# Optimization experiments

Hardware: AMD Instinct MI355X
Metric: run time of the kernel (lower is better)

Reference implementation:

```python
import jax, jax.numpy as jnp
import numpy as np

L, B, N, C, H = 8, 8, 512, 1024, 16
D = C // H
TP = (2.0 * D) ** 0.5  # temperature_coeff * head_dim, sqrt


def _ln(x):
    # LayerNorm(eps=1e-6, no affine)
    m = jnp.mean(x, axis=-1, keepdims=True)
    v = jnp.var(x, axis=-1, keepdims=True)
    return (x - m) * jax.lax.rsqrt(v + 1e-6)


def _modulate(x, shift, scale):
    return x * (1 + scale) + shift


def setup_inputs() -> dict:
    key = jax.random.key(0)
    ks = jax.random.split(key, 18)
    s = 0.02
    return {
        "x": jax.random.normal(ks[0], (B, N, C), dtype=jnp.float32),
        "time": jax.random.uniform(ks[1], (B, 1), dtype=jnp.float32) * 100.0,
        "label": jax.random.normal(ks[2], (B, 2), dtype=jnp.float32),
        "x_mask": jax.random.randint(ks[3], (B, N, 1), 0, 2).astype(jnp.float32),
        # ValueLabelEmbed: Linear(2 -> C)
        "Wl": jax.random.normal(ks[4], (C, 2), dtype=jnp.float32) * s,
        "bl": jnp.zeros((C,), dtype=jnp.float32),
        # per-layer stacked weights (leading dim L)
        "Wq": jax.random.normal(ks[5], (L, C, C), dtype=jnp.float32) * s,
        "Wk": jax.random.normal(ks[6], (L, C, C), dtype=jnp.float32) * s,
        "Wv": jax.random.normal(ks[7], (L, C, C), dtype=jnp.float32) * s,
        "W1": jax.random.normal(ks[8], (L, 4 * C, C), dtype=jnp.float32) * s,
        "b1": jnp.zeros((L, 4 * C), dtype=jnp.float32),
        "W2": jax.random.normal(ks[9], (L, C, 4 * C), dtype=jnp.float32) * s,
        "b2": jnp.zeros((L, C), dtype=jnp.float32),
        "Wm": jax.random.normal(ks[10], (L, 6 * C, C), dtype=jnp.float32) * s,
        "bm": jnp.zeros((L, 6 * C), dtype=jnp.float32),
        # FinalLayer
        "Wf": jax.random.normal(ks[11], (C, C), dtype=jnp.float32) * s,
        "bf": jnp.zeros((C,), dtype=jnp.float32),
        "Wmf": jax.random.normal(ks[12], (2 * C, C), dtype=jnp.float32) * s,
        "bmf": jnp.zeros((2 * C,), dtype=jnp.float32),
    }


def reference(x, time, label, x_mask, Wl, bl, Wq, Wk, Wv, W1, b1, W2, b2, Wm, bm, Wf, bf, Wmf, bmf):
    # ValueLabelEmbed: (B,2) -> (B,1,C)
    lemb = (label @ Wl.T + bl)[:, None, :]
    # TimeEmbedding: interleaved sin/cos of time / 10000^(2i/d)
    base = jnp.power(10000.0, 2.0 * jnp.arange(C, dtype=jnp.float32) / C)
    te = time / base  # (B, C)
    even = (jnp.arange(C) % 2) == 0
    te = jnp.where(even, jnp.sin(te), jnp.cos(te))
    c = lemb + te[:, None, :]  # (B,1,C)

    # self-attention mask: True where exactly one of the pair is valid
    xm = x_mask[:, :, 0]  # (B,N)
    mask = ((xm[:, :, None] + xm[:, None, :]) == 1.0)[:, None, :, :]  # (B,1,N,N)

    def block(xc, p):
        wq, wk, wv, w1, bb1, w2, bb2, wm, bbm = p
        m6 = jax.nn.selu(c) @ wm.T + bbm  # (B,1,6C)
        sm, sc, gm, sf, cf, gf = jnp.split(m6, 6, axis=-1)
        h = _modulate(_ln(xc), sm, sc) * x_mask
        q = (h @ wq.T).reshape(B, N, H, D)
        k = (h @ wk.T).reshape(B, N, H, D)
        v = (h @ wv.T).reshape(B, N, H, D)
        scores = jnp.einsum('bqhd,bkhd->bhqk', q, k) / TP
        scores = jnp.where(mask, -jnp.inf, scores)
        alpha = jax.nn.softmax(scores, axis=-1)
        att = jnp.einsum('bhqk,bkhd->bqhd', alpha, v).reshape(B, N, C)
        xc = xc + gm * att
        h2 = _modulate(_ln(xc), sf, cf)
        ffn = jax.nn.selu(h2 @ w1.T + bb1) @ w2.T + bb2
        xc = (xc + gf * ffn) * x_mask
        return xc, None

    x, _ = jax.lax.scan(block, x, (Wq, Wk, Wv, W1, b1, W2, b2, Wm, bm))

    # FinalLayer
    m2 = jax.nn.selu(c) @ Wmf.T + bmf
    shift, scale = jnp.split(m2, 2, axis=-1)
    out = (_modulate(_ln(x), shift, scale) @ Wf.T + bf) * x_mask
    return out
```

## Files before the change

kernel.cpp:

```cpp
#include <hip/hip_runtime.h>
#include <hip/hip_bf16.h>
#include <cstddef>

#define DEVI __device__ __forceinline__

typedef __attribute__((ext_vector_type(4))) float f4v;
typedef __attribute__((ext_vector_type(8))) short s8v;
typedef __attribute__((ext_vector_type(4))) short s4v;

using bf16 = __hip_bfloat16;

constexpr float SELU_A = 1.6732632423543772f;
constexpr float SELU_S = 1.0507009873554805f;
constexpr float TPINV  = 0.08838834764831845f;

DEVI float bfbits(short s) { return __uint_as_float(((unsigned)(unsigned short)s) << 16); }
DEVI unsigned short f2bu(float f) {
  bf16 h = __float2bfloat16(f);
  return __builtin_bit_cast(unsigned short, h);
}
DEVI float seluf(float x) { return x > 0.f ? SELU_S * x : SELU_S * SELU_A * (__expf(x) - 1.f); }

DEVI void gl16(const void* g, void* l) {
  __builtin_amdgcn_global_load_lds((__attribute__((address_space(1))) void*)g,
                                   (__attribute__((address_space(3))) void*)l, 16, 0, 0);
}

__global__ void k_compact(const float* __restrict__ xm, int* __restrict__ idx,
                          int* __restrict__ pos, int* __restrict__ cnt,
                          int* __restrict__ start, int* __restrict__ t2b)
{
  int t = threadIdx.x;
  int b = t >> 6, lane = t & 63;
  __shared__ int scnt[8];
  int base = b * 512 + lane * 8;
  int mb[8]; int lc = 0;
  #pragma unroll
  for (int i = 0; i < 8; i++) { mb[i] = (xm[base + i] != 0.f) ? 1 : 0; lc += mb[i]; }
  int s = lc;
  #pragma unroll
  for (int o = 1; o < 64; o <<= 1) { int tt = __shfl_up(s, o); if (lane >= o) s += tt; }
  int run = s - lc;
  #pragma unroll
  for (int i = 0; i < 8; i++) {
    int n = lane * 8 + i;
    if (mb[i]) { idx[b * 512 + run] = n; pos[b * 512 + n] = run; run++; }
    else pos[b * 512 + n] = -1;
  }
  if (lane == 63) scnt[b] = s;
  __syncthreads();
  if (t == 0) {
    int st = 0, tile = 0;
    for (int bb = 0; bb < 8; bb++) {
      cnt[bb] = scnt[bb];
      start[bb] = st;
      int nt = (scnt[bb] + 127) >> 7;
      for (int k = 0; k < nt; k++) t2b[tile++] = bb;
      st += nt * 128;
    }
    start[8] = st;
    for (; tile < 32; tile++) t2b[tile] = 0;
  }
}

__global__ __launch_bounds__(256) void k_gather(const float* __restrict__ xin,
    const int* __restrict__ idx, const int* __restrict__ cnt,
    const int* __restrict__ start, const int* __restrict__ t2b,
    float* __restrict__ xc)
{
  int row = blockIdx.x, t = threadIdx.x;
  if (row >= start[8]) return;
  int tb = t2b[row >> 7], slot = row - start[tb];
  f4v v = {0.f, 0.f, 0.f, 0.f};
  if (slot < cnt[tb])
    v = *(const f4v*)&xin[((size_t)tb * 512 + idx[tb * 512 + slot]) * 1024 + t * 4];
  *(f4v*)&xc[(size_t)row * 1024 + t * 4] = v;
}

__global__ __launch_bounds__(256) void k_scatter(const float* __restrict__ ffin,
    const int* __restrict__ pos, const int* __restrict__ start, float* __restrict__ out)
{
  int row = blockIdx.x, t = threadIdx.x, b = row >> 9;
  int p = pos[row];
  f4v v = {0.f, 0.f, 0.f, 0.f};
  if (p >= 0) v = *(const f4v*)&ffin[(size_t)(start[b] + p) * 1024 + t * 4];
  *(f4v*)&out[(size_t)row * 1024 + t * 4] = v;
}

__global__ __launch_bounds__(256) void k_conv(const float* __restrict__ src,
                                              bf16* __restrict__ dst, int n8)
{
  int i = blockIdx.x * 256 + threadIdx.x;
  if (i >= n8) return;
  const float* s = src + (size_t)i * 8;
  f4v a = *(const f4v*)s;
  f4v b = *(const f4v*)(s + 4);
  s8v o;
  #pragma unroll
  for (int j = 0; j < 4; j++) { o[j] = (short)f2bu(a[j]); o[4 + j] = (short)f2bu(b[j]); }
  *(s8v*)(dst + (size_t)i * 8) = o;
}

__global__ __launch_bounds__(256) void k_convall(
    const float* __restrict__ wq, const float* __restrict__ wk, const float* __restrict__ wv,
    const float* __restrict__ w1, const float* __restrict__ w2,
    bf16* __restrict__ wqkvb, bf16* __restrict__ w1b, bf16* __restrict__ w2b)
{
  int i = blockIdx.x * 256 + threadIdx.x;
  const float* src; bf16* dst;
  if (i < 393216) {
    int o = i * 8;
    int row = o >> 10, col = o & 1023;
    int sel = row >> 10, sr = row & 1023;
    src = (sel == 0 ? wq : sel == 1 ? wk : wv) + (size_t)sr * 1024 + col;
    dst = wqkvb + o;
  } else if (i < 917504) {
    size_t o = (size_t)(i - 393216) * 8;
    src = w1 + o; dst = w1b + o;
  } else if (i < 1441792) {
    size_t o = (size_t)(i - 917504) * 8;
    src = w2 + o; dst = w2b + o;
  } else return;
  f4v a = *(const f4v*)src;
  f4v b = *(const f4v*)(src + 4);
  s8v out;
  #pragma unroll
  for (int j = 0; j < 4; j++) { out[j] = (short)f2bu(a[j]); out[4 + j] = (short)f2bu(b[j]); }
  *(s8v*)dst = out;
}

__global__ void k_cond(const float* __restrict__ tim, const float* __restrict__ lab,
                       const float* __restrict__ Wl, const float* __restrict__ bl,
                       float* __restrict__ cs)
{
  int b = blockIdx.x, t = threadIdx.x;
  float l0 = lab[b * 2 + 0], l1 = lab[b * 2 + 1], tv = tim[b];
  #pragma unroll
  for (int i = 0; i < 4; i++) {
    int j = t + 256 * i;
    float e = powf(10000.f, (2.f * (float)j) * (1.f / 1024.f));
    float arg = tv / e;
    float te = ((j & 1) == 0) ? sinf(arg) : cosf(arg);
    float c = l0 * Wl[j * 2 + 0] + l1 * Wl[j * 2 + 1] + bl[j] + te;
    cs[b * 1024 + j] = seluf(c);
  }
}

__global__ __launch_bounds__(256) void k_small(
    const float* __restrict__ cs, const float* __restrict__ W, const float* __restrict__ bias,
    float* __restrict__ out, int O, int mode)
{
  __shared__ float cls[8192];
  int t = threadIdx.x;
  #pragma unroll
  for (int i = 0; i < 8; i++)
    *(f4v*)&cls[i * 1024 + t * 4] = *(const f4v*)&cs[i * 1024 + t * 4];
  __syncthreads();
  int w = t >> 6, l = t & 63;
  int o = blockIdx.x * 4 + w;
  if (o >= O) return;
  float acc[8] = {0.f, 0.f, 0.f, 0.f, 0.f, 0.f, 0.f, 0.f};
  const float* Wr = W + (size_t)o * 1024;
  for (int i = 0; i < 16; i++) {
    int k = i * 64 + l;
    float wv = Wr[k];
    #pragma unroll
    for (int b = 0; b < 8; b++) acc[b] += wv * cls[b * 1024 + k];
  }
  #pragma unroll
  for (int b = 0; b < 8; b++) {
    #pragma unroll
    for (int off = 32; off; off >>= 1) acc[b] += __shfl_xor(acc[b], off);
  }
  float bv = bias[o];
  #pragma unroll
  for (int b = 0; b < 8; b++) {
    if (l == b) {
      float val = acc[b] + bv;
      size_t dst;
      if (mode == 0) { int ll = o / 6144, ft = o - ll * 6144; dst = ((size_t)ll * 8 + b) * 6144 + ft; }
      else dst = (size_t)b * 2048 + o;
      out[dst] = val;
    }
  }
}

__global__ __launch_bounds__(256) void k_lnmod(
    const float* __restrict__ x, const float* __restrict__ shiftB, const float* __restrict__ scaleB,
    int bstride, const int* __restrict__ cnt, const int* __restrict__ start,
    const int* __restrict__ t2b, bf16* __restrict__ out)
{
  int row = blockIdx.x, t = threadIdx.x;
  if (row >= start[8]) return;
  int tb = t2b[row >> 7], slot = row - start[tb];
  if (slot >= cnt[tb]) {
    s4v z = {0, 0, 0, 0};
    *(s4v*)&out[(size_t)row * 1024 + t * 4] = z;
    return;
  }
  const float* xr = x + (size_t)row * 1024;
  f4v v = *(const f4v*)&xr[t * 4];
  float s = v[0] + v[1] + v[2] + v[3];
  float ss = v[0]*v[0] + v[1]*v[1] + v[2]*v[2] + v[3]*v[3];
  #pragma unroll
  for (int off = 32; off; off >>= 1) { s += __shfl_xor(s, off); ss += __shfl_xor(ss, off); }
  __shared__ float rs[4], rss[4];
  int w = t >> 6;
  if ((t & 63) == 0) { rs[w] = s; rss[w] = ss; }
  __syncthreads();
  s = rs[0] + rs[1] + rs[2] + rs[3];
  ss = rss[0] + rss[1] + rss[2] + rss[3];
  float mean = s * (1.f / 1024.f);
  float var = ss * (1.f / 1024.f) - mean * mean;
  float rstd = rsqrtf(var + 1e-6f);
  f4v sh = *(const f4v*)&shiftB[(size_t)tb * bstride + t * 4];
  f4v sc = *(const f4v*)&scaleB[(size_t)tb * bstride + t * 4];
  s4v o;
  #pragma unroll
  for (int i = 0; i < 4; i++)
    o[i] = (short)f2bu((v[i] - mean) * rstd * (1.f + sc[i]) + sh[i]);
  *(s4v*)&out[(size_t)row * 1024 + t * 4] = o;
}

__global__ __launch_bounds__(256) void k_resid(
    float* __restrict__ x, const bf16* __restrict__ att, const float* __restrict__ m6b,
    const int* __restrict__ cnt, const int* __restrict__ start,
    const int* __restrict__ t2b, bf16* __restrict__ h2)
{
  int row = blockIdx.x, t = threadIdx.x;
  if (row >= start[8]) return;
  int tb = t2b[row >> 7], slot = row - start[tb];
  if (slot >= cnt[tb]) {
    s4v z = {0, 0, 0, 0};
    *(s4v*)&h2[(size_t)row * 1024 + t * 4] = z;
    return;
  }
  float* xr = x + (size_t)row * 1024;
  const float* gm = m6b + (size_t)tb * 6144 + 2048;
  const float* sf = m6b + (size_t)tb * 6144 + 3072;
  const float* cf = m6b + (size_t)tb * 6144 + 4096;
  f4v xv = *(const f4v*)&xr[t * 4];
  s4v av = *(const s4v*)&att[((size_t)tb * 512 + slot) * 1024 + t * 4];
  f4v gv = *(const f4v*)&gm[t * 4];
  f4v vv;
  #pragma unroll
  for (int i = 0; i < 4; i++) vv[i] = xv[i] + gv[i] * bfbits(av[i]);
  *(f4v*)&xr[t * 4] = vv;
  float s = vv[0] + vv[1] + vv[2] + vv[3];
  float ss = vv[0]*vv[0] + vv[1]*vv[1] + vv[2]*vv[2] + vv[3]*vv[3];
  #pragma unroll
  for (int off = 32; off; off >>= 1) { s += __shfl_xor(s, off); ss += __shfl_xor(ss, off); }
  __shared__ float rs[4], rss[4];
  int w = t >> 6;
  if ((t & 63) == 0) { rs[w] = s; rss[w] = ss; }
  __syncthreads();
  s = rs[0] + rs[1] + rs[2] + rs[3];
  ss = rss[0] + rss[1] + rss[2] + rss[3];
  float mean = s * (1.f / 1024.f);
  float var = ss * (1.f / 1024.f) - mean * mean;
  float rstd = rsqrtf(var + 1e-6f);
  f4v sfv = *(const f4v*)&sf[t * 4];
  f4v cfv = *(const f4v*)&cf[t * 4];
  s4v o;
  #pragma unroll
  for (int i = 0; i < 4; i++)
    o[i] = (short)f2bu((vv[i] - mean) * rstd * (1.f + cfv[i]) + sfv[i]);
  *(s4v*)&h2[(size_t)row * 1024 + t * 4] = o;
}

__global__ __launch_bounds__(256) void k_attn(
    const bf16* __restrict__ q, const bf16* __restrict__ k, const bf16* __restrict__ vt,
    const int* __restrict__ cnt, bf16* __restrict__ att)
{
  int bh = blockIdx.y, b = bh >> 4, hh = bh & 15;
  int cntb = cnt[b];
  if ((int)blockIdx.x * 128 >= cntb) return;
  int t = threadIdx.x, w = t >> 6, lane = t & 63;
  int fr = lane & 15, g = lane >> 4;
  int qw = blockIdx.x * 128 + w * 32;
  const size_t ho = (size_t)bh * (512 * 64);

  __shared__ bf16 Pb[4][32][72];

  s8v qf[2][2];
  #pragma unroll
  for (int mf = 0; mf < 2; mf++)
    #pragma unroll
    for (int kk = 0; kk < 2; kk++)
      qf[mf][kk] = *(const s8v*)(q + ho + (size_t)(qw + mf * 16 + fr) * 64 + kk * 32 + g * 8);

  float mrow[2][4], lsum[2][4];
  f4v oacc[2][4];
  const f4v vzero = {0.f, 0.f, 0.f, 0.f};
  #pragma unroll
  for (int mf = 0; mf < 2; mf++)
    #pragma unroll
    for (int r = 0; r < 4; r++) { mrow[mf][r] = -3.0e38f; lsum[mf][r] = 0.f; }
  #pragma unroll
  for (int mf = 0; mf < 2; mf++)
    #pragma unroll
    for (int nd = 0; nd < 4; nd++) oacc[mf][nd] = vzero;

  int nkt = (cntb + 63) >> 6;
  for (int kt = 0; kt < nkt; kt++) {
    int kb0 = kt * 64;
    f4v sacc[2][4];
    #pragma unroll
    for (int mf = 0; mf < 2; mf++)
      #pragma unroll
      for (int nf = 0; nf < 4; nf++) sacc[mf][nf] = vzero;
    #pragma unroll
    for (int kk = 0; kk < 2; kk++) {
      s8v kf[4];
      #pragma unroll
      for (int nf = 0; nf < 4; nf++)
        kf[nf] = *(const s8v*)(k + ho + (size_t)(kb0 + nf * 16 + fr) * 64 + kk * 32 + g * 8);
      #pragma unroll
      for (int mf = 0; mf < 2; mf++)
        #pragma unroll
        for (int nf = 0; nf < 4; nf++)
          sacc[mf][nf] = __builtin_amdgcn_mfma_f32_16x16x32_bf16(qf[mf][kk], kf[nf], sacc[mf][nf], 0, 0, 0);
    }
    #pragma unroll
    for (int mf = 0; mf < 2; mf++) {
      #pragma unroll
      for (int r = 0; r < 4; r++) {
        float mx = -3.0e38f;
        #pragma unroll
        for (int nf = 0; nf < 4; nf++) {
          float s = sacc[mf][nf][r] * TPINV;
          if (kb0 + nf * 16 + fr >= cntb) s = -1.0e30f;
          sacc[mf][nf][r] = s;
          mx = fmaxf(mx, s);
        }
        mx = fmaxf(mx, __shfl_xor(mx, 1));
        mx = fmaxf(mx, __shfl_xor(mx, 2));
        mx = fmaxf(mx, __shfl_xor(mx, 4));
        mx = fmaxf(mx, __shfl_xor(mx, 8));
        float mnew = fmaxf(mrow[mf][r], mx);
        float corr = __expf(mrow[mf][r] - mnew);
        mrow[mf][r] = mnew;
        float ps = 0.f;
        #pragma unroll
        for (int nf = 0; nf < 4; nf++) {
          float p = __expf(sacc[mf][nf][r] - mnew);
          ps += p;
          Pb[w][mf * 16 + g * 4 + r][nf * 16 + fr] = __float2bfloat16(p);
        }
        lsum[mf][r] = lsum[mf][r] * corr + ps;
        #pragma unroll
        for (int nd = 0; nd < 4; nd++) oacc[mf][nd][r] *= corr;
      }
    }
    #pragma unroll
    for (int kk = 0; kk < 2; kk++) {
      s8v pf[2], vf[4];
      #pragma unroll
      for (int mf = 0; mf < 2; mf++)
        pf[mf] = *(const s8v*)&Pb[w][mf * 16 + fr][kk * 32 + g * 8];
      #pragma unroll
      for (int nd = 0; nd < 4; nd++)
        vf[nd] = *(const s8v*)(vt + ho + (size_t)(nd * 16 + fr) * 512 + kb0 + kk * 32 + g * 8);
      #pragma unroll
      for (int mf = 0; mf < 2; mf++)
        #pragma unroll
        for (int nd = 0; nd < 4; nd++)
          oacc[mf][nd] = __builtin_amdgcn_mfma_f32_16x16x32_bf16(pf[mf], vf[nd], oacc[mf][nd], 0, 0, 0);
    }
  }
  float inv[2][4];
  #pragma unroll
  for (int mf = 0; mf < 2; mf++)
    #pragma unroll
    for (int r = 0; r < 4; r++) {
      float ls = lsum[mf][r];
      ls += __shfl_xor(ls, 1);
      ls += __shfl_xor(ls, 2);
      ls += __shfl_xor(ls, 4);
      ls += __shfl_xor(ls, 8);
      inv[mf][r] = 1.f / ls;
    }
  #pragma unroll
  for (int mf = 0; mf < 2; mf++)
    #pragma unroll
    for (int nd = 0; nd < 4; nd++)
      #pragma unroll
      for (int r = 0; r < 4; r++) {
        int row = qw + mf * 16 + g * 4 + r;
        att[(size_t)(b * 512 + row) * 1024 + hh * 64 + nd * 16 + fr] =
            __float2bfloat16(oacc[mf][nd][r] * inv[mf][r]);
      }
}

template <int EPI, int BN>
__global__ __launch_bounds__(256) void k_gemm(
    const bf16* __restrict__ A, const bf16* __restrict__ W,
    const float* __restrict__ bias, int Kst, int kLen, int Ncols,
    const int* __restrict__ cnt, const int* __restrict__ start, const int* __restrict__ t2b,
    bf16* __restrict__ outb, float* __restrict__ outf,
    float* __restrict__ xio, const float* __restrict__ gfb)
{
  constexpr int FN = BN / 32;
  constexpr int NW = BN / 32;
  __shared__ bf16 As[128][64];
  __shared__ bf16 Ws[BN][64];
  int t = threadIdx.x, lane = t & 63, w = t >> 6;
  int wr = w >> 1, wc = w & 1;
  int m0 = blockIdx.y * 128, n0 = blockIdx.x * BN;
  if (m0 >= start[8]) return;
  int kOff = blockIdx.z * kLen;
  int fr = lane & 15, g = lane >> 4;

  const bf16* Abase = A + (size_t)m0 * Kst + kOff;
  const bf16* Wbase = W + (size_t)n0 * Kst + kOff;

  const f4v vzero = {0.f, 0.f, 0.f, 0.f};
  f4v acc[4][FN];
  #pragma unroll
  for (int i = 0; i < 4; i++)
    #pragma unroll
    for (int j = 0; j < FN; j++) acc[i][j] = vzero;

  int nkt = kLen >> 6;
  for (int kt = 0; kt < nkt; kt++) {
    int k0 = kt << 6;
    __syncthreads();
    #pragma unroll
    for (int i = 0; i < 4; i++) {
      int off = w * 4096 + i * 1024 + lane * 16;
      int row = off >> 7, ce = (off & 127) >> 1;
      gl16(Abase + (size_t)row * Kst + k0 + ce, (char*)As + w * 4096 + i * 1024);
    }
    #pragma unroll
    for (int i = 0; i < NW; i++) {
      int off = w * (NW * 1024) + i * 1024 + lane * 16;
      int row = off >> 7, ce = (off & 127) >> 1;
      gl16(Wbase + (size_t)row * Kst + k0 + ce, (char*)Ws + w * (NW * 1024) + i * 1024);
    }
    __syncthreads();
    #pragma unroll
    for (int kk = 0; kk < 2; kk++) {
      s8v af[4], bfr[FN];
      #pragma unroll
      for (int mf = 0; mf < 4; mf++)
        af[mf] = *(const s8v*)&As[wr * 64 + mf * 16 + fr][kk * 32 + g * 8];
      #pragma unroll
      for (int nf = 0; nf < FN; nf++)
        bfr[nf] = *(const s8v*)&Ws[wc * (BN / 2) + nf * 16 + fr][kk * 32 + g * 8];
      #pragma unroll
      for (int mf = 0; mf < 4; mf++)
        #pragma unroll
        for (int nf = 0; nf < FN; nf++)
          acc[mf][nf] = __builtin_amdgcn_mfma_f32_16x16x32_bf16(af[mf], bfr[nf], acc[mf][nf], 0, 0, 0);
    }
  }

  int tb = t2b[m0 >> 7];
  int sb = start[tb];
  int rq = (lane >> 4) * 4;
  #pragma unroll
  for (int mf = 0; mf < 4; mf++) {
    #pragma unroll
    for (int nf = 0; nf < FN; nf++) {
      int row0 = m0 + wr * 64 + mf * 16 + rq;
      int col = n0 + wc * (BN / 2) + nf * 16 + fr;
      if (EPI == 0) {
        int sel = col >> 10, cl = col & 1023;
        int nn = row0 - sb;
        int h2 = cl >> 6, dd = cl & 63;
        if (sel == 2) {
          s4v o4;
          #pragma unroll
          for (int r = 0; r < 4; r++) o4[r] = (short)f2bu(acc[mf][nf][r]);
          *(s4v*)&outb[(size_t)2 * 4194304 + (((size_t)tb * 16 + h2) * 64 + dd) * 512 + nn] = o4;
        } else {
          #pragma unroll
          for (int r = 0; r < 4; r++)
            outb[(size_t)sel * 4194304 + (((size_t)tb * 16 + h2) * 512 + (nn + r)) * 64 + dd] =
                __float2bfloat16(acc[mf][nf][r]);
        }
      } else {
        #pragma unroll
        for (int r = 0; r < 4; r++) {
          int row = row0 + r;
          float val = acc[mf][nf][r];
          if (EPI == 1) {
            outb[(size_t)row * Ncols + col] = __float2bfloat16(seluf(val + bias[col]));
          } else if (EPI == 2) {
            size_t idx = (size_t)row * 1024 + col;
            xio[idx] = xio[idx] + gfb[(size_t)tb * 6144 + col] * (val + bias[col]);
          } else if (EPI == 3) {
            outf[(size_t)row * 1024 + col] = val + bias[col];
          } else {
            outf[((size_t)blockIdx.z * 4096 + row) * 1024 + col] = val;
          }
        }
      }
    }
  }
}

__global__ __launch_bounds__(256) void k_comb(
    const float* __restrict__ part, const float* __restrict__ bias,
    const float* __restrict__ m6b, float* __restrict__ x,
    const int* __restrict__ cnt, const int* __restrict__ start, const int* __restrict__ t2b)
{
  int row = blockIdx.x, t = threadIdx.x;
  if (row >= start[8]) return;
  int tb = t2b[row >> 7], slot = row - start[tb];
  if (slot >= cnt[tb]) return;
  size_t o = (size_t)row * 1024 + t * 4;
  f4v s0 = *(const f4v*)&part[o];
  f4v s1 = *(const f4v*)&part[o + 4194304];
  f4v s2 = *(const f4v*)&part[o + 8388608];
  f4v s3 = *(const f4v*)&part[o + 12582912];
  f4v bv = *(const f4v*)&bias[t * 4];
  f4v gf = *(const f4v*)&m6b[(size_t)tb * 6144 + 5120 + t * 4];
  f4v xv = *(const f4v*)&x[o];
  #pragma unroll
  for (int i = 0; i < 4; i++)
    xv[i] = xv[i] + gf[i] * ((s0[i] + s1[i] + s2[i] + s3[i]) + bv[i]);
  *(f4v*)&x[o] = xv;
}

extern "C" void kernel_launch(void* const* d_in, const int* in_sizes, int n_in,
                              void* d_out, int out_size, void* d_ws, size_t ws_size,
                              hipStream_t stream)
{
  const float* x_in  = (const float*)d_in[0];
  const float* tim   = (const float*)d_in[1];
  const float* lab   = (const float*)d_in[2];
  const float* xmask = (const float*)d_in[3];
  const float* Wl  = (const float*)d_in[4];
  const float* bl  = (const float*)d_in[5];
  const float* Wq  = (const float*)d_in[6];
  const float* Wk  = (const float*)d_in[7];
  const float* Wv  = (const float*)d_in[8];
  const float* W1  = (const float*)d_in[9];
  const float* b1  = (const float*)d_in[10];
  const float* W2  = (const float*)d_in[11];
  const float* b2  = (const float*)d_in[12];
  const float* Wm  = (const float*)d_in[13];
  const float* bm  = (const float*)d_in[14];
  const float* Wf  = (const float*)d_in[15];
  const float* bfp = (const float*)d_in[16];
  const float* Wmf = (const float*)d_in[17];
  const float* bmf = (const float*)d_in[18];

  char* ws = (char*)d_ws;
  float* x     = (float*)(ws + 0);
  float* cs    = (float*)(ws + 16777216);
  float* mAll  = (float*)(ws + 16809984);
  float* m2v   = (float*)(ws + 18382848);
  bf16*  h     = (bf16*)(ws + 18448384);
  bf16*  qb    = (bf16*)(ws + 26836992);
  bf16*  kb    = (bf16*)(ws + 35225600);
  bf16*  vb    = (bf16*)(ws + 43614208);
  bf16*  att   = (bf16*)(ws + 52002816);
  bf16*  f1    = (bf16*)(ws + 60391424);
  bf16*  wqkvb = (bf16*)(ws + 93945856);
  bf16*  w1b   = (bf16*)(ws + 100237312);
  bf16*  w2b   = (bf16*)(ws + 108625920);
  bf16*  wfb   = (bf16*)(ws + 117014528);
  float* ffin  = (float*)(ws + 119111680);
  int*   idxb  = (int*)(ws + 135888896);
  int*   posb  = (int*)(ws + 135905280);
  int*   cntb  = (int*)(ws + 135921664);
  int*   strtb = (int*)(ws + 135921728);
  int*   t2bb  = (int*)(ws + 135921792);
  float* part  = (float*)(ws + 135921920);

  k_compact<<<1, 512, 0, stream>>>(xmask, idxb, posb, cntb, strtb, t2bb);
  k_gather<<<4096, 256, 0, stream>>>(x_in, idxb, cntb, strtb, t2bb, x);

  k_cond<<<8, 256, 0, stream>>>(tim, lab, Wl, bl, cs);
  k_small<<<12288, 256, 0, stream>>>(cs, Wm, bm, mAll, 49152, 0);
  k_small<<<512, 256, 0, stream>>>(cs, Wmf, bmf, m2v, 2048, 1);

  for (int l = 0; l < 8; l++) {
    const float* m6b = mAll + (size_t)l * 8 * 6144;
    k_convall<<<5632, 256, 0, stream>>>(Wq + (size_t)l * 1048576, Wk + (size_t)l * 1048576,
                                        Wv + (size_t)l * 1048576, W1 + (size_t)l * 4194304,
                                        W2 + (size_t)l * 4194304, wqkvb, w1b, w2b);

    k_lnmod<<<4096, 256, 0, stream>>>(x, m6b + 0, m6b + 1024, 6144, cntb, strtb, t2bb, h);
    k_gemm<0, 128><<<dim3(24, 32), 256, 0, stream>>>(h, wqkvb, nullptr, 1024, 1024, 3072,
                                                     cntb, strtb, t2bb,
                                                     qb, nullptr, nullptr, nullptr);
    k_attn<<<dim3(4, 128), 256, 0, stream>>>(qb, kb, vb, cntb, att);
    k_resid<<<4096, 256, 0, stream>>>(x, att, m6b, cntb, strtb, t2bb, h);
    k_gemm<1, 128><<<dim3(32, 32), 256, 0, stream>>>(h, w1b, b1 + l * 4096, 1024, 1024, 4096,
                                                     cntb, strtb, t2bb,
                                                     f1, nullptr, nullptr, nullptr);
    k_gemm<4, 64><<<dim3(16, 32, 4), 256, 0, stream>>>(f1, w2b, nullptr, 4096, 1024, 1024,
                                                       cntb, strtb, t2bb,
                                                       nullptr, part, nullptr, nullptr);
    k_comb<<<4096, 256, 0, stream>>>(part, b2 + l * 1024, m6b, x, cntb, strtb, t2bb);
  }

  k_conv<<<512, 256, 0, stream>>>(Wf, wfb, 131072);
  k_lnmod<<<4096, 256, 0, stream>>>(x, m2v + 0, m2v + 1024, 2048, cntb, strtb, t2bb, h);
  k_gemm<3, 64><<<dim3(16, 32), 256, 0, stream>>>(h, wfb, bfp, 1024, 1024, 1024,
                                                  cntb, strtb, t2bb,
                                                  nullptr, ffin, nullptr, nullptr);
  k_scatter<<<4096, 256, 0, stream>>>(ffin, posb, strtb, (float*)d_out);
}
```

Measured before the change: 1.640 ms.

## Overlap next-layer weight conversion with attention and fuse LN into FFN combine

Converts each next layer's fp32 weights to bf16 in extra blocks of the attention kernel, using double-buffered weight staging so the conversion overlaps attention instead of running as a separate launch. The FFN combine kernel now also computes the next LayerNorm-modulate, which removes the standalone lnmod launch and one pass over x. The split-K partials of the second FFN GEMM are stored as bf16 and use a wider N tile, reducing partial traffic at some accuracy cost. Dead epilogue code is also removed.

```diff
diff --git a/kernel.cpp b/kernel.cpp
--- a/kernel.cpp
+++ b/kernel.cpp
@@ -24,6 +24,15 @@
 DEVI void gl16(const void* g, void* l) {
   __builtin_amdgcn_global_load_lds((__attribute__((address_space(1))) void*)g,
                                    (__attribute__((address_space(3))) void*)l, 16, 0, 0);
+}
+
+DEVI void conv8(const float* __restrict__ src, bf16* __restrict__ dst) {
+  f4v a = *(const f4v*)src;
+  f4v b = *(const f4v*)(src + 4);
+  s8v o;
+  #pragma unroll
+  for (int j = 0; j < 4; j++) { o[j] = (short)f2bu(a[j]); o[4 + j] = (short)f2bu(b[j]); }
+  *(s8v*)dst = o;
 }
 
 __global__ void k_compact(const float* __restrict__ xm, int* __restrict__ idx,
@@ -87,46 +96,24 @@
   *(f4v*)&out[(size_t)row * 1024 + t * 4] = v;
 }
 
-__global__ __launch_bounds__(256) void k_conv(const float* __restrict__ src,
-                                              bf16* __restrict__ dst, int n8)
-{
-  int i = blockIdx.x * 256 + threadIdx.x;
-  if (i >= n8) return;
-  const float* s = src + (size_t)i * 8;
-  f4v a = *(const f4v*)s;
-  f4v b = *(const f4v*)(s + 4);
-  s8v o;
-  #pragma unroll
-  for (int j = 0; j < 4; j++) { o[j] = (short)f2bu(a[j]); o[4 + j] = (short)f2bu(b[j]); }
-  *(s8v*)(dst + (size_t)i * 8) = o;
-}
-
 __global__ __launch_bounds__(256) void k_convall(
     const float* __restrict__ wq, const float* __restrict__ wk, const float* __restrict__ wv,
     const float* __restrict__ w1, const float* __restrict__ w2,
     bf16* __restrict__ wqkvb, bf16* __restrict__ w1b, bf16* __restrict__ w2b)
 {
   int i = blockIdx.x * 256 + threadIdx.x;
-  const float* src; bf16* dst;
   if (i < 393216) {
     int o = i * 8;
     int row = o >> 10, col = o & 1023;
     int sel = row >> 10, sr = row & 1023;
-    src = (sel == 0 ? wq : sel == 1 ? wk : wv) + (size_t)sr * 1024 + col;
-    dst = wqkvb + o;
+    conv8((sel == 0 ? wq : sel == 1 ? wk : wv) + (size_t)sr * 1024 + col, wqkvb + o);
   } else if (i < 917504) {
     size_t o = (size_t)(i - 393216) * 8;
-    src = w1 + o; dst = w1b + o;
+    conv8(w1 + o, w1b + o);
   } else if (i < 1441792) {
     size_t o = (size_t)(i - 917504) * 8;
-    src = w2 + o; dst = w2b + o;
-  } else return;
-  f4v a = *(const f4v*)src;
-  f4v b = *(const f4v*)(src + 4);
-  s8v out;
-  #pragma unroll
-  for (int j = 0; j < 4; j++) { out[j] = (short)f2bu(a[j]); out[4 + j] = (short)f2bu(b[j]); }
-  *(s8v*)dst = out;
+    conv8(w2 + o, w2b + o);
+  }
 }
 
 __global__ void k_cond(const float* __restrict__ tim, const float* __restrict__ lab,
@@ -270,8 +257,37 @@
 
 __global__ __launch_bounds__(256) void k_attn(
     const bf16* __restrict__ q, const bf16* __restrict__ k, const bf16* __restrict__ vt,
-    const int* __restrict__ cnt, bf16* __restrict__ att)
-{
+    const int* __restrict__ cnt, bf16* __restrict__ att,
+    const float* __restrict__ nwq, const float* __restrict__ nwk, const float* __restrict__ nwv,
+    const float* __restrict__ nw1, const float* __restrict__ nw2,
+    bf16* __restrict__ dqkv, bf16* __restrict__ dw1, bf16* __restrict__ dw2, int mode)
+{
+  if (blockIdx.x >= 4) {
+    int cid = (blockIdx.x - 4) * 128 + blockIdx.y;
+    int i0 = cid * 256 + threadIdx.x;
+    #pragma unroll
+    for (int half = 0; half < 2; half++) {
+      int j = i0 * 2 + half;
+      if (mode == 1) {
+        if (j < 131072) conv8(nwq + (size_t)j * 8, dqkv + (size_t)j * 8);
+      } else {
+        if (j < 393216) {
+          int o = j * 8;
+          int row = o >> 10, col = o & 1023;
+          int sel = row >> 10, sr = row & 1023;
+          conv8((sel == 0 ? nwq : sel == 1 ? nwk : nwv) + (size_t)sr * 1024 + col, dqkv + o);
+        } else if (j < 917504) {
+          size_t o = (size_t)(j - 393216) * 8;
+          conv8(nw1 + o, dw1 + o);
+        } else {
+          size_t o = (size_t)(j - 917504) * 8;
+          conv8(nw2 + o, dw2 + o);
+        }
+      }
+    }
+    return;
+  }
+
   int bh = blockIdx.y, b = bh >> 4, hh = bh & 15;
   int cntb = cnt[b];
   if ((int)blockIdx.x * 128 >= cntb) return;
@@ -397,8 +413,7 @@
     const bf16* __restrict__ A, const bf16* __restrict__ W,
     const float* __restrict__ bias, int Kst, int kLen, int Ncols,
     const int* __restrict__ cnt, const int* __restrict__ start, const int* __restrict__ t2b,
-    bf16* __restrict__ outb, float* __restrict__ outf,
-    float* __restrict__ xio, const float* __restrict__ gfb)
+    bf16* __restrict__ outb, float* __restrict__ outf)
 {
   constexpr int FN = BN / 32;
   constexpr int NW = BN / 32;
@@ -486,13 +501,10 @@
           float val = acc[mf][nf][r];
           if (EPI == 1) {
             outb[(size_t)row * Ncols + col] = __float2bfloat16(seluf(val + bias[col]));
-          } else if (EPI == 2) {
-            size_t idx = (size_t)row * 1024 + col;
-            xio[idx] = xio[idx] + gfb[(size_t)tb * 6144 + col] * (val + bias[col]);
           } else if (EPI == 3) {
             outf[(size_t)row * 1024 + col] = val + bias[col];
           } else {
-            outf[((size_t)blockIdx.z * 4096 + row) * 1024 + col] = val;
+            outb[(size_t)blockIdx.z * 4194304 + (size_t)row * 1024 + col] = __float2bfloat16(val);
           }
         }
       }
@@ -501,26 +513,49 @@
 }
 
 __global__ __launch_bounds__(256) void k_comb(
-    const float* __restrict__ part, const float* __restrict__ bias,
-    const float* __restrict__ m6b, float* __restrict__ x,
-    const int* __restrict__ cnt, const int* __restrict__ start, const int* __restrict__ t2b)
+    const bf16* __restrict__ part, const float* __restrict__ bias,
+    const float* __restrict__ gfb, const float* __restrict__ shiftN,
+    const float* __restrict__ scaleN, int strideN,
+    float* __restrict__ x, const int* __restrict__ cnt, const int* __restrict__ start,
+    const int* __restrict__ t2b, bf16* __restrict__ h)
 {
   int row = blockIdx.x, t = threadIdx.x;
   if (row >= start[8]) return;
   int tb = t2b[row >> 7], slot = row - start[tb];
   if (slot >= cnt[tb]) return;
   size_t o = (size_t)row * 1024 + t * 4;
-  f4v s0 = *(const f4v*)&part[o];
-  f4v s1 = *(const f4v*)&part[o + 4194304];
-  f4v s2 = *(const f4v*)&part[o + 8388608];
-  f4v s3 = *(const f4v*)&part[o + 12582912];
+  s4v p0 = *(const s4v*)&part[o];
+  s4v p1 = *(const s4v*)&part[o + 4194304];
+  s4v p2 = *(const s4v*)&part[o + 8388608];
+  s4v p3 = *(const s4v*)&part[o + 12582912];
   f4v bv = *(const f4v*)&bias[t * 4];
-  f4v gf = *(const f4v*)&m6b[(size_t)tb * 6144 + 5120 + t * 4];
+  f4v gf = *(const f4v*)&gfb[(size_t)tb * 6144 + t * 4];
   f4v xv = *(const f4v*)&x[o];
+  f4v vv;
   #pragma unroll
   for (int i = 0; i < 4; i++)
-    xv[i] = xv[i] + gf[i] * ((s0[i] + s1[i] + s2[i] + s3[i]) + bv[i]);
-  *(f4v*)&x[o] = xv;
+    vv[i] = xv[i] + gf[i] * ((bfbits(p0[i]) + bfbits(p1[i]) + bfbits(p2[i]) + bfbits(p3[i])) + bv[i]);
+  *(f4v*)&x[o] = vv;
+  float s = vv[0] + vv[1] + vv[2] + vv[3];
+  float ss = vv[0]*vv[0] + vv[1]*vv[1] + vv[2]*vv[2] + vv[3]*vv[3];
+  #pragma unroll
+  for (int off = 32; off; off >>= 1) { s += __shfl_xor(s, off); ss += __shfl_xor(ss, off); }
+  __shared__ float rs[4], rss[4];
+  int w = t >> 6;
+  if ((t & 63) == 0) { rs[w] = s; rss[w] = ss; }
+  __syncthreads();
+  s = rs[0] + rs[1] + rs[2] + rs[3];
+  ss = rss[0] + rss[1] + rss[2] + rss[3];
+  float mean = s * (1.f / 1024.f);
+  float var = ss * (1.f / 1024.f) - mean * mean;
+  float rstd = rsqrtf(var + 1e-6f);
+  f4v sh = *(const f4v*)&shiftN[(size_t)tb * strideN + t * 4];
+  f4v sc = *(const f4v*)&scaleN[(size_t)tb * strideN + t * 4];
+  s4v ho;
+  #pragma unroll
+  for (int i = 0; i < 4; i++)
+    ho[i] = (short)f2bu((vv[i] - mean) * rstd * (1.f + sc[i]) + sh[i]);
+  *(s4v*)&h[(size_t)row * 1024 + t * 4] = ho;
 }
 
 extern "C" void kernel_launch(void* const* d_in, const int* in_sizes, int n_in,
@@ -558,9 +593,9 @@
   bf16*  vb    = (bf16*)(ws + 43614208);
   bf16*  att   = (bf16*)(ws + 52002816);
   bf16*  f1    = (bf16*)(ws + 60391424);
-  bf16*  wqkvb = (bf16*)(ws + 93945856);
-  bf16*  w1b   = (bf16*)(ws + 100237312);
-  bf16*  w2b   = (bf16*)(ws + 108625920);
+  bf16*  wqkv0 = (bf16*)(ws + 93945856);
+  bf16*  w1b0  = (bf16*)(ws + 100237312);
+  bf16*  w2b0  = (bf16*)(ws + 108625920);
   bf16*  wfb   = (bf16*)(ws + 117014528);
   float* ffin  = (float*)(ws + 119111680);
   int*   idxb  = (int*)(ws + 135888896);
@@ -568,7 +603,14 @@
   int*   cntb  = (int*)(ws + 135921664);
   int*   strtb = (int*)(ws + 135921728);
   int*   t2bb  = (int*)(ws + 135921792);
-  float* part  = (float*)(ws + 135921920);
+  bf16*  part  = (bf16*)(ws + 135921920);
+  bf16*  wqkv1 = (bf16*)(ws + 169476352);
+  bf16*  w1b1  = (bf16*)(ws + 175767808);
+  bf16*  w2b1  = (bf16*)(ws + 184156416);
+
+  bf16* wqkvS[2] = { wqkv0, wqkv1 };
+  bf16* w1S[2]   = { w1b0, w1b1 };
+  bf16* w2S[2]   = { w2b0, w2b1 };
 
   k_compact<<<1, 512, 0, stream>>>(xmask, idxb, posb, cntb, strtb, t2bb);
   k_gather<<<4096, 256, 0, stream>>>(x_in, idxb, cntb, strtb, t2bb, x);
@@ -577,31 +619,40 @@
   k_small<<<12288, 256, 0, stream>>>(cs, Wm, bm, mAll, 49152, 0);
   k_small<<<512, 256, 0, stream>>>(cs, Wmf, bmf, m2v, 2048, 1);
 
+  k_convall<<<5632, 256, 0, stream>>>(Wq, Wk, Wv, W1, W2, wqkv0, w1b0, w2b0);
+  k_lnmod<<<4096, 256, 0, stream>>>(x, mAll + 0, mAll + 1024, 6144, cntb, strtb, t2bb, h);
+
   for (int l = 0; l < 8; l++) {
-    const float* m6b = mAll + (size_t)l * 8 * 6144;
-    k_convall<<<5632, 256, 0, stream>>>(Wq + (size_t)l * 1048576, Wk + (size_t)l * 1048576,
-                                        Wv + (size_t)l * 1048576, W1 + (size_t)l * 4194304,
-                                        W2 + (size_t)l * 4194304, wqkvb, w1b, w2b);
-
-    k_lnmod<<<4096, 256, 0, stream>>>(x, m6b + 0, m6b + 1024, 6144, cntb, strtb, t2bb, h);
-    k_gemm<0, 128><<<dim3(24, 32), 256, 0, stream>>>(h, wqkvb, nullptr, 1024, 1024, 3072,
-                                                     cntb, strtb, t2bb,
-                                                     qb, nullptr, nullptr, nullptr);
-    k_attn<<<dim3(4, 128), 256, 0, stream>>>(qb, kb, vb, cntb, att);
+    const float* m6b = mAll + (size_t)l * 49152;
+    int sel = l & 1, nsel = sel ^ 1;
+    int last = (l == 7);
+
+    k_gemm<0, 128><<<dim3(24, 32), 256, 0, stream>>>(h, wqkvS[sel], nullptr, 1024, 1024, 3072,
+                                                     cntb, strtb, t2bb, qb, nullptr);
+    if (!last) {
+      k_attn<<<dim3(26, 128), 256, 0, stream>>>(qb, kb, vb, cntb, att,
+          Wq + (size_t)(l + 1) * 1048576, Wk + (size_t)(l + 1) * 1048576,
+          Wv + (size_t)(l + 1) * 1048576, W1 + (size_t)(l + 1) * 4194304,
+          W2 + (size_t)(l + 1) * 4194304,
+          wqkvS[nsel], w1S[nsel], w2S[nsel], 0);
+    } else {
+      k_attn<<<dim3(26, 128), 256, 0, stream>>>(qb, kb, vb, cntb, att,
+          Wf, Wf, Wf, Wf, Wf, wfb, wfb, wfb, 1);
+    }
     k_resid<<<4096, 256, 0, stream>>>(x, att, m6b, cntb, strtb, t2bb, h);
-    k_gemm<1, 128><<<dim3(32, 32), 256, 0, stream>>>(h, w1b, b1 + l * 4096, 1024, 1024, 4096,
-                                                     cntb, strtb, t2bb,
-                                                     f1, nullptr, nullptr, nullptr);
-    k_gemm<4, 64><<<dim3(16, 32, 4), 256, 0, stream>>>(f1, w2b, nullptr, 4096, 1024, 1024,
-                                                       cntb, strtb, t2bb,
-                                                       nullptr, part, nullptr, nullptr);
-    k_comb<<<4096, 256, 0, stream>>>(part, b2 + l * 1024, m6b, x, cntb, strtb, t2bb);
-  }
-
-  k_conv<<<512, 256, 0, stream>>>(Wf, wfb, 131072);
-  k_lnmod<<<4096, 256, 0, stream>>>(x, m2v + 0, m2v + 1024, 2048, cntb, strtb, t2bb, h);
+    k_gemm<1, 128><<<dim3(32, 32), 256, 0, stream>>>(h, w1S[sel], b1 + l * 4096, 1024, 1024, 4096,
+                                                     cntb, strtb, t2bb, f1, nullptr);
+    k_gemm<4, 128><<<dim3(8, 32, 4), 256, 0, stream>>>(f1, w2S[sel], nullptr, 4096, 1024, 1024,
+                                                       cntb, strtb, t2bb, part, nullptr);
+    const float* nShift = last ? m2v : (mAll + (size_t)(l + 1) * 49152);
+    const float* nScale = last ? (m2v + 1024) : (mAll + (size_t)(l + 1) * 49152 + 1024);
+    int nStride = last ? 2048 : 6144;
+    k_comb<<<4096, 256, 0, stream>>>(part, b2 + l * 1024, m6b + 5120,
+                                     nShift, nScale, nStride,
+                                     x, cntb, strtb, t2bb, h);
+  }
+
   k_gemm<3, 64><<<dim3(16, 32), 256, 0, stream>>>(h, wfb, bfp, 1024, 1024, 1024,
-                                                  cntb, strtb, t2bb,
-                                                  nullptr, ffin, nullptr, nullptr);
+                                                  cntb, strtb, t2bb, nullptr, ffin);
   k_scatter<<<4096, 256, 0, stream>>>(ffin, posb, strtb, (float*)d_out);
 }
```

New measurement: 1.630 ms. No clear change (-0.6%).
